# Kernel optimization log

Hardware: AMD Instinct MI355X
Metric: run time of the kernel (lower is better)

Reference implementation:

```python
import jax, jax.numpy as jnp
import numpy as np

N_HEAD = 8


def _ln(x, g, b, eps=1e-5):
    m = jnp.mean(x, -1, keepdims=True)
    v = jnp.mean((x - m) ** 2, -1, keepdims=True)
    return (x - m) * jax.lax.rsqrt(v + eps) * g + b


def setup_inputs() -> dict:
    key = jax.random.key(0)
    ks = jax.random.split(key, 8)
    B, S, H = 4, 2048, 1024
    PAD = 512  # trailing all-zero (padded) tokens -> masked keys via sign(sum|x|)==0
    s = 0.02
    x = jax.random.normal(ks[0], (B, S, H), jnp.float32)
    x = x.at[:, S - PAD:, :].set(0.0)
    return {
        "x": x,
        "in_w": jax.random.normal(ks[1], (3 * H, H), jnp.float32) * s,
        "in_b": jnp.zeros((3 * H,), jnp.float32),
        "out_w": jax.random.normal(ks[2], (H, H), jnp.float32) * s,
        "out_b": jnp.zeros((H,), jnp.float32),
        "fc1_w": jax.random.normal(ks[3], (H, H), jnp.float32) * s,
        "fc1_b": jnp.zeros((H,), jnp.float32),
        "fc2_w": jax.random.normal(ks[4], (H, H), jnp.float32) * s,
        "fc2_b": jnp.zeros((H,), jnp.float32),
        "g1": jnp.ones((H,), jnp.float32),
        "b1": jnp.zeros((H,), jnp.float32),
        "g2": jnp.ones((H,), jnp.float32),
        "b2": jnp.zeros((H,), jnp.float32),
    }


def reference(x, in_w, in_b, out_w, out_b, fc1_w, fc1_b, fc2_w, fc2_b, g1, b1, g2, b2):
    B, S, H = x.shape
    d = H // N_HEAD
    # key padding mask (real_time=False path): key masked where sign(sum|x|)==0
    pad = jnp.sum(jnp.abs(x), axis=-1) == 0  # [B, S]
    # fused qkv projection (torch MultiheadAttention in_proj)
    qkv = x @ in_w.T + in_b  # [B, S, 3H]
    q, k, v = jnp.split(qkv, 3, axis=-1)
    to_heads = lambda t: t.reshape(B, S, N_HEAD, d).transpose(0, 2, 1, 3)  # [B,h,S,d]
    q, k, v = to_heads(q), to_heads(k), to_heads(v)
    scale = 1.0 / jnp.sqrt(jnp.asarray(d, x.dtype))
    scores = jnp.einsum('bhqd,bhkd->bhqk', q, k) * scale  # [B,h,S,S]
    scores = jnp.where(pad[:, None, None, :], -jnp.inf, scores)
    attn = jax.nn.softmax(scores, axis=-1)
    ctx = jnp.einsum('bhqk,bhkd->bhqd', attn, v)
    ctx = ctx.transpose(0, 2, 1, 3).reshape(B, S, H)
    attn_out = ctx @ out_w.T + out_b
    x1 = _ln(attn_out + x, g1, b1)
    ff = jax.nn.relu(x1 @ fc1_w.T + fc1_b) @ fc2_w.T + fc2_b
    return _ln(ff + x1, g2, b2)
```

## Files before the change

kernel.cpp:

```cpp
#include <hip/hip_runtime.h>
#include <cstdint>
#include <cstddef>

#define B_ 4
#define S_ 2048
#define H_ 1024
#define NH 8
#define HD 128
#define MROWS (B_ * S_)

typedef unsigned short u16;
typedef __bf16 bf16x8 __attribute__((ext_vector_type(8)));
typedef float f32x4 __attribute__((ext_vector_type(4)));
typedef float f32x16 __attribute__((ext_vector_type(16)));
typedef unsigned int u32x4 __attribute__((ext_vector_type(4)));

__device__ __forceinline__ u16 f2b(float f) {
    unsigned u = __builtin_bit_cast(unsigned, f);
    u += 0x7FFFu + ((u >> 16) & 1u);
    return (u16)(u >> 16);
}
__device__ __forceinline__ float b2f(u16 h) {
    unsigned u = ((unsigned)h) << 16;
    return __builtin_bit_cast(float, u);
}
__device__ __forceinline__ unsigned cvtpk(float lo, float hi) {
    unsigned r;
    asm("v_cvt_pk_bf16_f32 %0, %1, %2" : "=v"(r) : "v"(lo), "v"(hi));
    return r;
}
__device__ __forceinline__ void perm32(unsigned& a, unsigned& b) {
    asm("v_permlane32_swap_b32 %0, %1" : "+v"(a), "+v"(b));
}

__device__ __forceinline__ void llds16(const void* g, void* l) {
    __builtin_amdgcn_global_load_lds(
        (const __attribute__((address_space(1))) unsigned int*)g,
        (__attribute__((address_space(3))) unsigned int*)l,
        16, 0, 0);
}

__device__ __forceinline__ bf16x8 ld16(const u16* p) {
    return *(const bf16x8*)p;
}

__device__ __forceinline__ f32x4 mfma_bf16(bf16x8 a, bf16x8 b, f32x4 c) {
    return __builtin_amdgcn_mfma_f32_16x16x32_bf16(a, b, c, 0, 0, 0);
}
__device__ __forceinline__ f32x16 mfma32(bf16x8 a, bf16x8 b, f32x16 c) {
    return __builtin_amdgcn_mfma_f32_32x32x16_bf16(a, b, c, 0, 0, 0);
}

__global__ void k_f2b_all(const float* __restrict__ w0, const float* __restrict__ w1,
                          const float* __restrict__ w2, const float* __restrict__ w3,
                          u16* __restrict__ o0, u16* __restrict__ o1,
                          u16* __restrict__ o2, u16* __restrict__ o3) {
    int i = blockIdx.x * 256 + threadIdx.x;
    const float* src;
    u16* dst;
    if (i < 786432) { src = w0; dst = o0; }
    else if (i < 1048576) { src = w1; dst = o1; i -= 786432; }
    else if (i < 1310720) { src = w2; dst = o2; i -= 1048576; }
    else { src = w3; dst = o3; i -= 1310720; }
    float4 v = ((const float4*)src)[i];
    uint2 o;
    o.x = cvtpk(v.x, v.y);
    o.y = cvtpk(v.z, v.w);
    ((uint2*)dst)[i] = o;
}

__global__ void k_xconv(const float* __restrict__ x, u16* __restrict__ xb,
                        float* __restrict__ maskf) {
    const int row = blockIdx.x, t = threadIdx.x;
    float4 v = ((const float4*)(x + (size_t)row * H_))[t];
    uint2 o;
    o.x = cvtpk(v.x, v.y);
    o.y = cvtpk(v.z, v.w);
    ((uint2*)(xb + (size_t)row * H_))[t] = o;
    float sa = fabsf(v.x) + fabsf(v.y) + fabsf(v.z) + fabsf(v.w);
    for (int off = 32; off; off >>= 1) sa += __shfl_xor(sa, off);
    __shared__ float red[4];
    if ((t & 63) == 0) red[t >> 6] = sa;
    __syncthreads();
    if (t == 0)
        maskf[row] = ((red[0] + red[1] + red[2] + red[3]) == 0.0f) ? -1e30f : 0.0f;
}

__global__ void k_tiles(const float* __restrict__ maskf, int* __restrict__ tlist,
                        int* __restrict__ ntl) {
    __shared__ int cnt[4][32];
    const int tid = threadIdx.x;
    if (tid < 128) {
        const int b = tid >> 5, t = tid & 31;
        const float* m = maskf + b * S_ + t * 64;
        int c = 0;
        for (int i = 0; i < 64; ++i) c += (m[i] == 0.0f);
        cnt[b][t] = c;
    }
    __syncthreads();
    if (tid < 4) {
        int n = 0;
        for (int t = 0; t < 32; ++t) {
            const int c = cnt[tid][t];
            if (c) tlist[tid * 32 + n++] = t | ((c < 64) ? 0x10000 : 0);
        }
        ntl[tid] = n;
    }
}

template <int MODE>
__global__ __launch_bounds__(256, 2) void k_gemm(
    const u16* __restrict__ A, const u16* __restrict__ Bw,
    const float* __restrict__ bias, int N, int K,
    u16* __restrict__ C, u16* __restrict__ qb, u16* __restrict__ kb,
    u16* __restrict__ vT) {
    __shared__ __align__(16) u16 lds[2][2 * 128 * 64];
    const int tid = threadIdx.x;
    const int wave = tid >> 6, lane = tid & 63;
    const int bn = blockIdx.x, bm = blockIdx.y;
    const int wr = wave >> 1, wc = wave & 1;
    const int r = lane & 15, g = lane >> 4;

    f32x4 acc[4][4];
#pragma unroll
    for (int m = 0; m < 4; ++m)
#pragma unroll
        for (int n = 0; n < 4; ++n) acc[m][n] = (f32x4){0.f, 0.f, 0.f, 0.f};

    const u16* Abase = A + (size_t)bm * 128 * K;
    const u16* Bbase = Bw + (size_t)bn * 128 * K;

    auto stage = [&](int buf, int k0) {
        u16* As = &lds[buf][0];
        u16* Bs = &lds[buf][8192];
#pragma unroll
        for (int i = 0; i < 4; ++i) {
            const int chunk = i * 256 + tid;
            const int row = chunk >> 3;
            const int slot = chunk & 7;
            const int gq = slot ^ (row & 7);
            llds16(Abase + (size_t)row * K + k0 + gq * 8,
                   As + (i * 256 + wave * 64) * 8);
            llds16(Bbase + (size_t)row * K + k0 + gq * 8,
                   Bs + (i * 256 + wave * 64) * 8);
        }
    };

    stage(0, 0);
    __syncthreads();
    int cur = 0;
    for (int k0 = 0; k0 < K; k0 += 64) {
        if (k0 + 64 < K) stage(cur ^ 1, k0 + 64);
        const u16* As = &lds[cur][0];
        const u16* Bs = &lds[cur][8192];

        bf16x8 af[2][4], bf[2][4];
#pragma unroll
        for (int ks = 0; ks < 2; ++ks) {
#pragma unroll
            for (int m = 0; m < 4; ++m) {
                const int row = wr * 64 + m * 16 + r;
                const int q = (ks * 4 + g) ^ (r & 7);
                af[ks][m] = ld16(As + row * 64 + q * 8);
            }
#pragma unroll
            for (int n = 0; n < 4; ++n) {
                const int row = wc * 64 + n * 16 + r;
                const int q = (ks * 4 + g) ^ (r & 7);
                bf[ks][n] = ld16(Bs + row * 64 + q * 8);
            }
        }
#pragma unroll
        for (int ks = 0; ks < 2; ++ks)
#pragma unroll
            for (int m = 0; m < 4; ++m)
#pragma unroll
                for (int n = 0; n < 4; ++n)
                    acc[m][n] = mfma_bf16(af[ks][m], bf[ks][n], acc[m][n]);

        __syncthreads();
        cur ^= 1;
    }

    if constexpr (MODE == 2) {
        const int part = bn >> 3;
        const int h = bn & 7;
        const float qs = 1.4426950408889634f * 0.08838834764831845f;
#pragma unroll
        for (int n = 0; n < 4; ++n) {
            const int dd = wc * 64 + n * 16 + r;
            const float bv = bias[bn * 128 + dd];
#pragma unroll
            for (int m = 0; m < 4; ++m) {
                const int rm = bm * 128 + wr * 64 + m * 16 + g * 4;
                const int b = rm >> 11;
                const int s0r = rm & 2047;
#pragma unroll
                for (int i = 0; i < 4; ++i) {
                    float v = acc[m][n][i] + bv;
                    if (part == 0) {
                        qb[(((size_t)b * NH + h) * S_ + (s0r + i)) * HD + dd] =
                            f2b(v * qs);
                    } else if (part == 1) {
                        kb[(((size_t)b * NH + h) * S_ + (s0r + i)) * HD + dd] = f2b(v);
                    } else {
                        vT[(((size_t)b * NH + h) * HD + dd) * S_ + (s0r + i)] = f2b(v);
                    }
                }
            }
        }
    } else {
#pragma unroll
        for (int n = 0; n < 4; ++n) {
            const int cn = bn * 128 + wc * 64 + n * 16 + r;
            const float bv = bias[cn];
#pragma unroll
            for (int m = 0; m < 4; ++m) {
                const int rm = bm * 128 + wr * 64 + m * 16 + g * 4;
#pragma unroll
                for (int i = 0; i < 4; ++i) {
                    float v = acc[m][n][i] + bv;
                    if (MODE == 1) v = fmaxf(v, 0.f);
                    C[(size_t)(rm + i) * N + cn] = f2b(v);
                }
            }
        }
    }
}

__global__ __launch_bounds__(256, 2) void k_attn(
    const u16* __restrict__ qb, const u16* __restrict__ kb,
    const u16* __restrict__ vT, const float* __restrict__ maskf,
    const int* __restrict__ tlist, const int* __restrict__ ntl,
    u16* __restrict__ ctxb) {
    __shared__ __align__(16) u16 lds[2][16384];
    const int qt = blockIdx.x, bh = blockIdx.y;
    const int b = bh >> 3, h = bh & 7;
    const int tid = threadIdx.x;
    const int w = tid >> 6, lane = tid & 63;
    const int c = lane & 31, hi = lane >> 5;
    const int q0 = qt * 128 + w * 32;

    const u16* Qp = qb + ((size_t)bh * S_ + q0) * HD;
    const u16* Kp = kb + (size_t)bh * S_ * HD;
    const u16* Vp = vT + (size_t)bh * HD * S_;
    const float* mrow = maskf + b * S_;
    const int* tl = tlist + b * 32;
    const int nt = ntl[b];

    bf16x8 qf[8];
#pragma unroll
    for (int ds = 0; ds < 8; ++ds) qf[ds] = ld16(Qp + c * HD + ds * 16 + hi * 8);

    f32x16 ctx[4];
#pragma unroll
    for (int d4 = 0; d4 < 4; ++d4)
#pragma unroll
        for (int i = 0; i < 16; ++i) ctx[d4][i] = 0.f;
    float mrun = -1e30f, lrun = 0.f;

    auto stage = [&](int buf, int t) {
        const int k0 = t * 64;
        u16* Kt = &lds[buf][0];
        u16* Vt = &lds[buf][8192];
#pragma unroll
        for (int i = 0; i < 4; ++i) {
            const int call = w * 4 + i;
            const int row = call * 4 + (lane >> 4);
            const int sg = (lane & 15) ^ (row & 7);
            llds16(Kp + (size_t)(k0 + row) * HD + sg * 8, Kt + call * 512);
        }
#pragma unroll
        for (int i = 0; i < 4; ++i) {
            const int call = w * 4 + i;
            const int row = call * 8 + (lane >> 3);
            const int sg = (lane & 7) ^ (row & 7);
            llds16(Vp + (size_t)row * S_ + k0 + sg * 8, Vt + call * 512);
        }
    };

    int cur = 0;
    stage(0, tl[0] & 0xFFFF);
    __syncthreads();

    for (int j = 0; j < nt; ++j) {
        if (j + 1 < nt) stage(cur ^ 1, tl[j + 1] & 0xFFFF);
        const int ent = tl[j];
        const int k0 = (ent & 0xFFFF) * 64;
        const u16* Kt = &lds[cur][0];
        const u16* Vt = &lds[cur][8192];

        f32x16 p[2];
#pragma unroll
        for (int kk = 0; kk < 2; ++kk)
#pragma unroll
            for (int i = 0; i < 16; ++i) p[kk][i] = 0.f;
        __builtin_amdgcn_s_setprio(1);
#pragma unroll
        for (int kk = 0; kk < 2; ++kk) {
            const int rk = kk * 32 + c;
            const int sw = rk & 7;
#pragma unroll
            for (int ds = 0; ds < 8; ++ds) {
                bf16x8 kf = ld16(Kt + rk * 128 + ((ds * 2 + hi) ^ sw) * 8);
                p[kk] = mfma32(kf, qf[ds], p[kk]);
            }
        }
        __builtin_amdgcn_s_setprio(0);

        if (ent & 0x10000) {
#pragma unroll
            for (int kk = 0; kk < 2; ++kk)
#pragma unroll
                for (int qd = 0; qd < 4; ++qd) {
                    f32x4 mk = *(const f32x4*)(mrow + k0 + kk * 32 + qd * 8 + hi * 4);
#pragma unroll
                    for (int i = 0; i < 4; ++i) p[kk][qd * 4 + i] += mk[i];
                }
        }

        float t8[8];
#pragma unroll
        for (int i = 0; i < 8; ++i)
            t8[i] = fmaxf(fmaxf(p[0][i], p[0][i + 8]),
                          fmaxf(p[1][i], p[1][i + 8]));
        float t4a = fmaxf(t8[0], t8[4]), t4b = fmaxf(t8[1], t8[5]);
        float t4c = fmaxf(t8[2], t8[6]), t4d = fmaxf(t8[3], t8[7]);
        float pmax = fmaxf(fmaxf(t4a, t4b), fmaxf(t4c, t4d));
        pmax = fmaxf(pmax, __shfl_xor(pmax, 32));

        if (!__all(pmax - mrun <= 8.0f)) {
            const float mn = fmaxf(mrun, pmax);
            const float al = exp2f(mrun - mn);
            lrun *= al;
#pragma unroll
            for (int d4 = 0; d4 < 4; ++d4)
#pragma unroll
                for (int i = 0; i < 16; ++i) ctx[d4][i] *= al;
            mrun = mn;
        }

#pragma unroll
        for (int kk = 0; kk < 2; ++kk)
#pragma unroll
            for (int i = 0; i < 16; ++i) p[kk][i] = exp2f(p[kk][i] - mrun);
        float s8[8];
#pragma unroll
        for (int i = 0; i < 8; ++i)
            s8[i] = (p[0][i] + p[0][i + 8]) + (p[1][i] + p[1][i + 8]);
        float ls = ((s8[0] + s8[4]) + (s8[1] + s8[5])) +
                   ((s8[2] + s8[6]) + (s8[3] + s8[7]));
        ls += __shfl_xor(ls, 32);
        lrun += ls;

        unsigned pk[16];
#pragma unroll
        for (int kk = 0; kk < 2; ++kk)
#pragma unroll
            for (int pp = 0; pp < 8; ++pp)
                pk[kk * 8 + pp] = cvtpk(p[kk][2 * pp], p[kk][2 * pp + 1]);

        bf16x8 pb[4];
#pragma unroll
        for (int ks = 0; ks < 4; ++ks) {
            const int o = (ks >> 1) * 8 + (ks & 1) * 4;
            unsigned a0 = pk[o + 0], b0 = pk[o + 2];
            unsigned a1 = pk[o + 1], b1 = pk[o + 3];
            perm32(a0, b0);
            perm32(a1, b1);
            u32x4 dw;
            dw[0] = a0; dw[1] = a1; dw[2] = b0; dw[3] = b1;
            pb[ks] = __builtin_bit_cast(bf16x8, dw);
        }

        __builtin_amdgcn_s_setprio(1);
#pragma unroll
        for (int d4 = 0; d4 < 4; ++d4) {
            const int rd = d4 * 32 + c;
            const int sw = rd & 7;
#pragma unroll
            for (int ks = 0; ks < 4; ++ks) {
                bf16x8 vf = ld16(Vt + rd * 64 + ((ks * 2 + hi) ^ sw) * 8);
                ctx[d4] = mfma32(vf, pb[ks], ctx[d4]);
            }
        }
        __builtin_amdgcn_s_setprio(0);
        __syncthreads();
        cur ^= 1;
    }

    const float inv = 1.0f / lrun;
    u16* cw = &lds[0][0] + w * 4352;
#pragma unroll
    for (int d4 = 0; d4 < 4; ++d4)
#pragma unroll
        for (int qd = 0; qd < 4; ++qd) {
            unsigned lo = cvtpk(ctx[d4][qd * 4 + 0] * inv, ctx[d4][qd * 4 + 1] * inv);
            unsigned hi2 = cvtpk(ctx[d4][qd * 4 + 2] * inv, ctx[d4][qd * 4 + 3] * inv);
            unsigned long long pv = ((unsigned long long)hi2 << 32) | lo;
            *(unsigned long long*)(cw + c * 136 + d4 * 32 + qd * 8 + hi * 4) = pv;
        }
    __syncthreads();
    const int row = lane >> 1, part = lane & 1;
    const u16* src = cw + row * 136 + part * 64;
    u16* dst = ctxb + ((size_t)b * S_ + q0 + row) * H_ + h * HD + part * 64;
#pragma unroll
    for (int u = 0; u < 8; ++u)
        *(u32x4*)(dst + u * 8) = *(const u32x4*)(src + u * 8);
}

template <int OUT_BF16>
__global__ void k_ln(const u16* __restrict__ a, const u16* __restrict__ res,
                     const float* __restrict__ gam, const float* __restrict__ bet,
                     void* __restrict__ out) {
    const int row = blockIdx.x, t = threadIdx.x;
    float v[4];
    ushort4 av = ((const ushort4*)(a + (size_t)row * H_))[t];
    ushort4 rv = ((const ushort4*)(res + (size_t)row * H_))[t];
    v[0] = b2f(av.x) + b2f(rv.x);
    v[1] = b2f(av.y) + b2f(rv.y);
    v[2] = b2f(av.z) + b2f(rv.z);
    v[3] = b2f(av.w) + b2f(rv.w);
    float s = v[0] + v[1] + v[2] + v[3];
    float q = v[0] * v[0] + v[1] * v[1] + v[2] * v[2] + v[3] * v[3];
    for (int off = 32; off; off >>= 1) {
        s += __shfl_xor(s, off);
        q += __shfl_xor(q, off);
    }
    __shared__ float red[8];
    if ((t & 63) == 0) {
        red[t >> 6] = s;
        red[4 + (t >> 6)] = q;
    }
    __syncthreads();
    s = red[0] + red[1] + red[2] + red[3];
    q = red[4] + red[5] + red[6] + red[7];
    const float mean = s * (1.f / 1024.f);
    const float var = q * (1.f / 1024.f) - mean * mean;
    const float rinv = rsqrtf(var + 1e-5f);
    float4 gv = ((const float4*)gam)[t];
    float4 bv = ((const float4*)bet)[t];
    float o0 = (v[0] - mean) * rinv * gv.x + bv.x;
    float o1 = (v[1] - mean) * rinv * gv.y + bv.y;
    float o2 = (v[2] - mean) * rinv * gv.z + bv.z;
    float o3 = (v[3] - mean) * rinv * gv.w + bv.w;
    if constexpr (OUT_BF16) {
        uint2 o;
        o.x = cvtpk(o0, o1);
        o.y = cvtpk(o2, o3);
        ((uint2*)((u16*)out + (size_t)row * H_))[t] = o;
    } else {
        float4 o;
        o.x = o0; o.y = o1; o.z = o2; o.w = o3;
        ((float4*)((float*)out + (size_t)row * H_))[t] = o;
    }
}

extern "C" void kernel_launch(void* const* d_in, const int* in_sizes, int n_in,
                              void* d_out, int out_size, void* d_ws, size_t ws_size,
                              hipStream_t stream) {
    const float* x     = (const float*)d_in[0];
    const float* in_w  = (const float*)d_in[1];
    const float* in_b  = (const float*)d_in[2];
    const float* out_w = (const float*)d_in[3];
    const float* out_b = (const float*)d_in[4];
    const float* fc1_w = (const float*)d_in[5];
    const float* fc1_b = (const float*)d_in[6];
    const float* fc2_w = (const float*)d_in[7];
    const float* fc2_b = (const float*)d_in[8];
    const float* g1    = (const float*)d_in[9];
    const float* b1    = (const float*)d_in[10];
    const float* g2    = (const float*)d_in[11];
    const float* b2    = (const float*)d_in[12];

    char* p = (char*)d_ws;
    auto take = [&](size_t bytes) {
        char* q = p;
        p += (bytes + 255) & ~(size_t)255;
        return (void*)q;
    };
    u16* wqkv    = (u16*)take((size_t)3 * H_ * H_ * 2);
    u16* wout    = (u16*)take((size_t)H_ * H_ * 2);
    u16* wfc1    = (u16*)take((size_t)H_ * H_ * 2);
    u16* wfc2    = (u16*)take((size_t)H_ * H_ * 2);
    float* maskf = (float*)take((size_t)MROWS * 4);
    int* tlist   = (int*)take(4 * 32 * sizeof(int));
    int* ntl     = (int*)take(4 * sizeof(int));
    const size_t actb = (size_t)MROWS * H_ * 2;
    u16* regA = (u16*)take(actb);
    u16* regB = (u16*)take(actb);
    u16* regC = (u16*)take(actb);
    u16* regD = (u16*)take(actb);
    u16* regE = (u16*)take(actb);
    u16* regF = (u16*)take(actb);

    k_f2b_all<<<6144, 256, 0, stream>>>(in_w, out_w, fc1_w, fc2_w,
                                        wqkv, wout, wfc1, wfc2);
    k_xconv<<<MROWS, 256, 0, stream>>>(x, regA, maskf);
    k_tiles<<<1, 128, 0, stream>>>(maskf, tlist, ntl);

    k_gemm<2><<<dim3(24, 64), 256, 0, stream>>>(regA, wqkv, in_b, 3 * H_, H_,
                                                nullptr, regB, regC, regD);
    k_attn<<<dim3(16, 32), 256, 0, stream>>>(regB, regC, regD, maskf, tlist, ntl,
                                             regE);
    k_gemm<0><<<dim3(8, 64), 256, 0, stream>>>(regE, wout, out_b, H_, H_, regB,
                                               nullptr, nullptr, nullptr);
    k_ln<1><<<MROWS, 256, 0, stream>>>(regB, regA, g1, b1, regF);
    k_gemm<1><<<dim3(8, 64), 256, 0, stream>>>(regF, wfc1, fc1_b, H_, H_, regC,
                                               nullptr, nullptr, nullptr);
    k_gemm<0><<<dim3(8, 64), 256, 0, stream>>>(regC, wfc2, fc2_b, H_, H_, regD,
                                               nullptr, nullptr, nullptr);
    k_ln<0><<<MROWS, 256, 0, stream>>>(regD, regF, g2, b2, (float*)d_out);
}
```

Measured before the change: 278.8 us.

## Rework GEMM into 128x256 tiles with triple-buffered K=32 pipeline

The bf16 GEMM kernel changes from 128x128 tiles with a double-buffered K=64 loop to 128x256 tiles, where each wave owns a 64-column strip over all 128 rows. It uses a three-stage LDS ring with K=32 steps and explicit vmcnt waits, and interleaves the async global-to-LDS prefetches between the MFMA groups with s_setprio. The aim is to raise data reuse per tile, hide load latency better and cut the number of barriers per FLOP. In exchange it doubles the accumulator registers and halves the grid size, which risks lower occupancy or spills and fewer workgroups to fill the CUs.

New measurement: 284.3 us. No clear change (+2.0%).

```diff
diff --git a/kernel.cpp b/kernel.cpp
--- a/kernel.cpp
+++ b/kernel.cpp
@@ -114,85 +114,115 @@
     const float* __restrict__ bias, int N, int K,
     u16* __restrict__ C, u16* __restrict__ qb, u16* __restrict__ kb,
     u16* __restrict__ vT) {
-    __shared__ __align__(16) u16 lds[2][2 * 128 * 64];
+    __shared__ __align__(16) u16 lds[3][12288];
     const int tid = threadIdx.x;
-    const int wave = tid >> 6, lane = tid & 63;
+    const int w = tid >> 6, lane = tid & 63;
+    const int r = lane & 15, g = lane >> 4;
     const int bn = blockIdx.x, bm = blockIdx.y;
-    const int wr = wave >> 1, wc = wave & 1;
-    const int r = lane & 15, g = lane >> 4;
-
-    f32x4 acc[4][4];
-#pragma unroll
-    for (int m = 0; m < 4; ++m)
+    const int NT = K >> 5;
+
+    const u16* Ab = A + (size_t)bm * 128 * K;
+    const u16* Bb = Bw + (size_t)bn * 256 * K;
+
+    const u16* sA[2];
+    const u16* sB[4];
+#pragma unroll
+    for (int i = 0; i < 2; ++i) {
+        const int c = i * 256 + tid;
+        const int row = c >> 2;
+        const int p = (c & 3) ^ ((row >> 1) & 3);
+        sA[i] = Ab + (size_t)row * K + p * 8;
+    }
+#pragma unroll
+    for (int i = 0; i < 4; ++i) {
+        const int c = i * 256 + tid;
+        const int row = c >> 2;
+        const int p = (c & 3) ^ ((row >> 1) & 3);
+        sB[i] = Bb + (size_t)row * K + p * 8;
+    }
+
+    f32x4 acc[8][4];
+#pragma unroll
+    for (int m = 0; m < 8; ++m)
 #pragma unroll
         for (int n = 0; n < 4; ++n) acc[m][n] = (f32x4){0.f, 0.f, 0.f, 0.f};
 
-    const u16* Abase = A + (size_t)bm * 128 * K;
-    const u16* Bbase = Bw + (size_t)bn * 128 * K;
-
-    auto stage = [&](int buf, int k0) {
-        u16* As = &lds[buf][0];
-        u16* Bs = &lds[buf][8192];
-#pragma unroll
-        for (int i = 0; i < 4; ++i) {
-            const int chunk = i * 256 + tid;
-            const int row = chunk >> 3;
-            const int slot = chunk & 7;
-            const int gq = slot ^ (row & 7);
-            llds16(Abase + (size_t)row * K + k0 + gq * 8,
-                   As + (i * 256 + wave * 64) * 8);
-            llds16(Bbase + (size_t)row * K + k0 + gq * 8,
-                   Bs + (i * 256 + wave * 64) * 8);
-        }
-    };
-
-    stage(0, 0);
-    __syncthreads();
-    int cur = 0;
-    for (int k0 = 0; k0 < K; k0 += 64) {
-        if (k0 + 64 < K) stage(cur ^ 1, k0 + 64);
-        const u16* As = &lds[cur][0];
-        const u16* Bs = &lds[cur][8192];
-
-        bf16x8 af[2][4], bf[2][4];
-#pragma unroll
-        for (int ks = 0; ks < 2; ++ks) {
-#pragma unroll
-            for (int m = 0; m < 4; ++m) {
-                const int row = wr * 64 + m * 16 + r;
-                const int q = (ks * 4 + g) ^ (r & 7);
-                af[ks][m] = ld16(As + row * 64 + q * 8);
-            }
-#pragma unroll
-            for (int n = 0; n < 4; ++n) {
-                const int row = wc * 64 + n * 16 + r;
-                const int q = (ks * 4 + g) ^ (r & 7);
-                bf[ks][n] = ld16(Bs + row * 64 + q * 8);
-            }
-        }
-#pragma unroll
-        for (int ks = 0; ks < 2; ++ks)
-#pragma unroll
-            for (int m = 0; m < 4; ++m)
-#pragma unroll
-                for (int n = 0; n < 4; ++n)
-                    acc[m][n] = mfma_bf16(af[ks][m], bf[ks][n], acc[m][n]);
-
-        __syncthreads();
-        cur ^= 1;
+    const int xga = g ^ ((r >> 1) & 3);
+    const int aoff = r * 32 + xga * 8;
+    const int boff = w * 2048 + r * 32 + xga * 8;
+
+#pragma unroll
+    for (int i = 0; i < 2; ++i) llds16(sA[i], &lds[0][0] + (i * 256 + w * 64) * 8);
+#pragma unroll
+    for (int i = 0; i < 4; ++i) llds16(sB[i], &lds[0][4096] + (i * 256 + w * 64) * 8);
+#pragma unroll
+    for (int i = 0; i < 2; ++i) llds16(sA[i] + 32, &lds[1][0] + (i * 256 + w * 64) * 8);
+#pragma unroll
+    for (int i = 0; i < 4; ++i) llds16(sB[i] + 32, &lds[1][4096] + (i * 256 + w * 64) * 8);
+
+    int bcur = 0, bstage = 2;
+    for (int t = 0; t < NT; ++t) {
+        if (t + 1 < NT) asm volatile("s_waitcnt vmcnt(6)" ::: "memory");
+        else            asm volatile("s_waitcnt vmcnt(0)" ::: "memory");
+        __builtin_amdgcn_sched_barrier(0);
+        __builtin_amdgcn_s_barrier();
+        __builtin_amdgcn_sched_barrier(0);
+        const u16* As = &lds[bcur][0];
+        const u16* Bs = &lds[bcur][4096];
+        u16* Ad = &lds[bstage][0];
+        u16* Bd = &lds[bstage][4096];
+        const int kk = (t + 2) * 32;
+        const bool pf = (t + 2) < NT;
+
+        bf16x8 af[4], bf[4];
+#pragma unroll
+        for (int n = 0; n < 4; ++n) bf[n] = ld16(Bs + n * 512 + boff);
+#pragma unroll
+        for (int m = 0; m < 4; ++m) af[m] = ld16(As + m * 512 + aoff);
+        if (pf) {
+            llds16(sA[0] + kk, Ad + (w * 64) * 8);
+            llds16(sA[1] + kk, Ad + (256 + w * 64) * 8);
+            llds16(sB[0] + kk, Bd + (w * 64) * 8);
+        }
+        __builtin_amdgcn_s_setprio(1);
+#pragma unroll
+        for (int m = 0; m < 4; ++m)
+#pragma unroll
+            for (int n = 0; n < 4; ++n)
+                acc[m][n] = mfma_bf16(af[m], bf[n], acc[m][n]);
+        __builtin_amdgcn_s_setprio(0);
+
+#pragma unroll
+        for (int m = 0; m < 4; ++m) af[m] = ld16(As + (m + 4) * 512 + aoff);
+        if (pf) {
+            llds16(sB[1] + kk, Bd + (256 + w * 64) * 8);
+            llds16(sB[2] + kk, Bd + (512 + w * 64) * 8);
+            llds16(sB[3] + kk, Bd + (768 + w * 64) * 8);
+        }
+        __builtin_amdgcn_s_setprio(1);
+#pragma unroll
+        for (int m = 0; m < 4; ++m)
+#pragma unroll
+            for (int n = 0; n < 4; ++n)
+                acc[m + 4][n] = mfma_bf16(af[m], bf[n], acc[m + 4][n]);
+        __builtin_amdgcn_s_setprio(0);
+
+        bcur = (bcur == 2) ? 0 : bcur + 1;
+        bstage = (bstage == 2) ? 0 : bstage + 1;
     }
 
     if constexpr (MODE == 2) {
-        const int part = bn >> 3;
-        const int h = bn & 7;
         const float qs = 1.4426950408889634f * 0.08838834764831845f;
 #pragma unroll
         for (int n = 0; n < 4; ++n) {
-            const int dd = wc * 64 + n * 16 + r;
-            const float bv = bias[bn * 128 + dd];
-#pragma unroll
-            for (int m = 0; m < 4; ++m) {
-                const int rm = bm * 128 + wr * 64 + m * 16 + g * 4;
+            const int col = bn * 256 + w * 64 + n * 16 + r;
+            const int part = col >> 10;
+            const int h = (col >> 7) & 7;
+            const int dd = col & 127;
+            const float bv = bias[col];
+#pragma unroll
+            for (int m = 0; m < 8; ++m) {
+                const int rm = bm * 128 + m * 16 + g * 4;
                 const int b = rm >> 11;
                 const int s0r = rm & 2047;
 #pragma unroll
@@ -212,16 +242,16 @@
     } else {
 #pragma unroll
         for (int n = 0; n < 4; ++n) {
-            const int cn = bn * 128 + wc * 64 + n * 16 + r;
-            const float bv = bias[cn];
-#pragma unroll
-            for (int m = 0; m < 4; ++m) {
-                const int rm = bm * 128 + wr * 64 + m * 16 + g * 4;
+            const int col = bn * 256 + w * 64 + n * 16 + r;
+            const float bv = bias[col];
+#pragma unroll
+            for (int m = 0; m < 8; ++m) {
+                const int rm = bm * 128 + m * 16 + g * 4;
 #pragma unroll
                 for (int i = 0; i < 4; ++i) {
                     float v = acc[m][n][i] + bv;
                     if (MODE == 1) v = fmaxf(v, 0.f);
-                    C[(size_t)(rm + i) * N + cn] = f2b(v);
+                    C[(size_t)(rm + i) * N + col] = f2b(v);
                 }
             }
         }
@@ -499,16 +529,16 @@
     k_xconv<<<MROWS, 256, 0, stream>>>(x, regA, maskf);
     k_tiles<<<1, 128, 0, stream>>>(maskf, tlist, ntl);
 
-    k_gemm<2><<<dim3(24, 64), 256, 0, stream>>>(regA, wqkv, in_b, 3 * H_, H_,
+    k_gemm<2><<<dim3(12, 64), 256, 0, stream>>>(regA, wqkv, in_b, 3 * H_, H_,
                                                 nullptr, regB, regC, regD);
     k_attn<<<dim3(16, 32), 256, 0, stream>>>(regB, regC, regD, maskf, tlist, ntl,
                                              regE);
-    k_gemm<0><<<dim3(8, 64), 256, 0, stream>>>(regE, wout, out_b, H_, H_, regB,
+    k_gemm<0><<<dim3(4, 64), 256, 0, stream>>>(regE, wout, out_b, H_, H_, regB,
                                                nullptr, nullptr, nullptr);
     k_ln<1><<<MROWS, 256, 0, stream>>>(regB, regA, g1, b1, regF);
-    k_gemm<1><<<dim3(8, 64), 256, 0, stream>>>(regF, wfc1, fc1_b, H_, H_, regC,
+    k_gemm<1><<<dim3(4, 64), 256, 0, stream>>>(regF, wfc1, fc1_b, H_, H_, regC,
                                                nullptr, nullptr, nullptr);
-    k_gemm<0><<<dim3(8, 64), 256, 0, stream>>>(regC, wfc2, fc2_b, H_, H_, regD,
+    k_gemm<0><<<dim3(4, 64), 256, 0, stream>>>(regC, wfc2, fc2_b, H_, H_, regD,
                                                nullptr, nullptr, nullptr);
     k_ln<0><<<MROWS, 256, 0, stream>>>(regD, regF, g2, b2, (float*)d_out);
 }
```
